# Kernel tuning notes

Measured on AMD Instinct MI355X. Metric: run time of the kernel, lower is better.

The kernel has to match this reference:

```python
import jax, jax.numpy as jnp
import numpy as np

IN_CH, OUT_CH, MINI = 1024, 1024, 8
GY, GX = OUT_CH // MINI, IN_CH // MINI  # 128, 128
BATCH = 32768


def setup_inputs() -> dict:
    key = jax.random.key(0)
    k1, k2 = jax.random.split(key)
    x = jax.random.normal(k1, (BATCH, IN_CH), dtype=jnp.float32)
    # kaiming-style init scale for the eigens parameter
    eigens = jax.random.normal(k2, (GY, GX, MINI), dtype=jnp.float32) * (2.0 / (GX * MINI)) ** 0.5
    return {"x": x, "eigens": eigens}


def reference(x, eigens):
    # Block-circulant linear: for each (y, x_blk) grid cell, circularly convolve
    # the length-MINI eigen vector with the corresponding input block, then sum
    # over input blocks. Done in the frequency domain (full FFT, matching
    # torch.rfft(..., onesided=False) + complex_mult + irfft in the original),
    # but with the redundant gridDim_y repeat fused into a complex einsum.
    gy, gx, k = eigens.shape
    xb = x.reshape(-1, gx, k)                      # [B, GX, K]
    f_e = jnp.fft.fft(eigens, axis=-1)             # [GY, GX, K] complex
    f_x = jnp.fft.fft(xb, axis=-1)                 # [B, GX, K] complex
    f_out = jnp.einsum('yxk,bxk->byk', f_e, f_x)   # elementwise mult + sum over GX
    out = jnp.fft.ifft(f_out, axis=-1).real.astype(x.dtype)  # [B, GY, K]
    return out.reshape(-1, gy * k)                 # [B, OUT_CH]
```

## Files before the change

kernel.cpp:

```cpp
#include <hip/hip_runtime.h>
#include <stdint.h>

#define M_BATCH 32768
#define N_OUT   1024
#define K_IN    1024

#define BM 128
#define BN 128
#define BK 64

typedef __attribute__((ext_vector_type(8))) short  short8;
typedef __attribute__((ext_vector_type(4))) float  f32x4;

__device__ __forceinline__ unsigned short f2bf(float f) {
    __bf16 h = (__bf16)f;
    return __builtin_bit_cast(unsigned short, h);
}

__global__ __launch_bounds__(256) void build_w(const float* __restrict__ eig,
                                               unsigned short* __restrict__ W) {
    int tid = blockIdx.x * 256 + threadIdx.x;
    int y  = tid >> 7;
    int xb = tid & 127;
    const float* e = eig + (size_t)((y << 7) + xb) * 8;
    f32x4 e0 = *reinterpret_cast<const f32x4*>(e);
    f32x4 e1 = *reinterpret_cast<const f32x4*>(e + 4);
    float ev[8] = {e0[0], e0[1], e0[2], e0[3], e1[0], e1[1], e1[2], e1[3]};
#pragma unroll
    for (int j = 0; j < 8; ++j) {
        alignas(16) unsigned short wv[8];
#pragma unroll
        for (int c = 0; c < 8; ++c) wv[c] = f2bf(ev[(j - c) & 7]);
        *reinterpret_cast<uint4*>(W + (size_t)(y * 8 + j) * K_IN + xb * 8) =
            *reinterpret_cast<const uint4*>(wv);
    }
}

__global__ __launch_bounds__(256) void gemm_bt(const float* __restrict__ A,
                                               const unsigned short* __restrict__ W,
                                               float* __restrict__ C) {
    __shared__ unsigned short Alds[BM * BK];
    __shared__ unsigned short Blds[BN * BK];

    const int bid  = blockIdx.x;
    const int swz  = (bid & 7) * 256 + (bid >> 3);
    const int nblk = swz & 7;
    const int mblk = swz >> 3;
    const int brow = mblk * BM;
    const int bcol = nblk * BN;

    const int tid  = threadIdx.x;
    const int lane = tid & 63;
    const int wv   = tid >> 6;
    const int wm   = wv >> 1;
    const int wn   = wv & 1;

    f32x4 acc[4][4];
    const f32x4 zero = {0.f, 0.f, 0.f, 0.f};
#pragma unroll
    for (int i = 0; i < 4; ++i)
#pragma unroll
        for (int j = 0; j < 4; ++j) acc[i][j] = zero;

    const int srow  = tid >> 3;
    const int sslot = tid & 7;
    const int sk8   = sslot ^ (srow & 7);
    const float*          Abase = A + (size_t)(brow + srow) * K_IN + sk8 * 8;
    const unsigned short* Wbase = W + (size_t)(bcol + srow) * K_IN + sk8 * 8;
    unsigned short* AldsW = Alds + srow * BK + sslot * 8;
    unsigned short* BldsW = Blds + srow * BK + sslot * 8;

    for (int kt = 0; kt < K_IN; kt += BK) {
        __syncthreads();
#pragma unroll
        for (int it = 0; it < 4; ++it) {
            const float* src = Abase + (size_t)it * 32 * K_IN + kt;
            f32x4 v0 = *reinterpret_cast<const f32x4*>(src);
            f32x4 v1 = *reinterpret_cast<const f32x4*>(src + 4);
            short8 b;
#pragma unroll
            for (int i = 0; i < 4; ++i) b[i]     = (short)f2bf(v0[i]);
#pragma unroll
            for (int i = 0; i < 4; ++i) b[i + 4] = (short)f2bf(v1[i]);
            *reinterpret_cast<short8*>(AldsW + it * 32 * BK) = b;
        }
#pragma unroll
        for (int it = 0; it < 4; ++it) {
            const unsigned short* src = Wbase + (size_t)it * 32 * K_IN + kt;
            short8 b = *reinterpret_cast<const short8*>(src);
            *reinterpret_cast<short8*>(BldsW + it * 32 * BK) = b;
        }
        __syncthreads();
#pragma unroll
        for (int ks = 0; ks < 2; ++ks) {
            short8 af[4], bfr[4];
            const int cb = ks * 4 + (lane >> 4);
#pragma unroll
            for (int mt = 0; mt < 4; ++mt) {
                int row  = wm * 64 + mt * 16 + (lane & 15);
                int slot = cb ^ (row & 7);
                af[mt] = *reinterpret_cast<const short8*>(Alds + row * BK + slot * 8);
            }
#pragma unroll
            for (int nt = 0; nt < 4; ++nt) {
                int row  = wn * 64 + nt * 16 + (lane & 15);
                int slot = cb ^ (row & 7);
                bfr[nt] = *reinterpret_cast<const short8*>(Blds + row * BK + slot * 8);
            }
#pragma unroll
            for (int mt = 0; mt < 4; ++mt)
#pragma unroll
                for (int nt = 0; nt < 4; ++nt)
                    acc[mt][nt] = __builtin_amdgcn_mfma_f32_16x16x32_bf16(
                        af[mt], bfr[nt], acc[mt][nt], 0, 0, 0);
        }
    }

#pragma unroll
    for (int mt = 0; mt < 4; ++mt) {
#pragma unroll
        for (int nt = 0; nt < 4; ++nt) {
            int col = bcol + wn * 64 + nt * 16 + (lane & 15);
#pragma unroll
            for (int r = 0; r < 4; ++r) {
                int row = brow + wm * 64 + mt * 16 + (lane >> 4) * 4 + r;
                C[(size_t)row * N_OUT + col] = acc[mt][nt][r];
            }
        }
    }
}

extern "C" void kernel_launch(void* const* d_in, const int* in_sizes, int n_in,
                              void* d_out, int out_size, void* d_ws, size_t ws_size,
                              hipStream_t stream) {
    const float* x   = (const float*)d_in[0];
    const float* eig = (const float*)d_in[1];
    float* out = (float*)d_out;
    unsigned short* W = (unsigned short*)d_ws;
    if (ws_size < (size_t)N_OUT * K_IN * sizeof(unsigned short)) return;

    hipLaunchKernelGGL(build_w, dim3((16384 + 255) / 256), dim3(256), 0, stream,
                       eig, W);
    hipLaunchKernelGGL(gemm_bt, dim3((M_BATCH / BM) * (N_OUT / BN)), dim3(256),
                       0, stream, x, W, out);
}
```

Baseline: 329.8 us.

## Pre-convert x to bf16 and load GEMM tiles directly into LDS

Adds a separate pass that converts x from fp32 to bf16 in workspace. A new GEMM kernel then uses global_load_lds to copy bf16 tiles for both operands straight into shared memory, replacing the register-staged fp32 load and in-loop conversion. This cuts the GEMM's A-operand traffic and its conversion work, at the cost of an extra full read and write of x. The path only runs when the workspace is large enough; otherwise it falls back to the old kernel.

New measurement: 298.2 us. -9.6%, faster.

```diff
diff --git a/kernel.cpp b/kernel.cpp
--- a/kernel.cpp
+++ b/kernel.cpp
@@ -15,6 +15,29 @@
 __device__ __forceinline__ unsigned short f2bf(float f) {
     __bf16 h = (__bf16)f;
     return __builtin_bit_cast(unsigned short, h);
+}
+
+typedef const __attribute__((address_space(1))) unsigned int* gas_ptr;
+typedef __attribute__((address_space(3))) unsigned int*       las_ptr;
+
+__device__ __forceinline__ void gload_lds16(const void* g, void* l) {
+    __builtin_amdgcn_global_load_lds((gas_ptr)g, (las_ptr)l, 16, 0, 0);
+}
+
+__global__ __launch_bounds__(256) void cvt_x(const float* __restrict__ x,
+                                             unsigned short* __restrict__ xb) {
+    const size_t total8 = (size_t)M_BATCH * K_IN / 8;
+    const size_t stride = (size_t)gridDim.x * 256;
+    for (size_t i = (size_t)blockIdx.x * 256 + threadIdx.x; i < total8; i += stride) {
+        f32x4 v0 = *reinterpret_cast<const f32x4*>(x + i * 8);
+        f32x4 v1 = *reinterpret_cast<const f32x4*>(x + i * 8 + 4);
+        short8 b;
+#pragma unroll
+        for (int j = 0; j < 4; ++j) b[j]     = (short)f2bf(v0[j]);
+#pragma unroll
+        for (int j = 0; j < 4; ++j) b[j + 4] = (short)f2bf(v1[j]);
+        *reinterpret_cast<short8*>(xb + i * 8) = b;
+    }
 }
 
 __global__ __launch_bounds__(256) void build_w(const float* __restrict__ eig,
@@ -36,6 +59,87 @@
     }
 }
 
+__global__ __launch_bounds__(256) void gemm_bf16(const unsigned short* __restrict__ A,
+                                                 const unsigned short* __restrict__ W,
+                                                 float* __restrict__ C) {
+    __shared__ unsigned short Alds[BM * BK];
+    __shared__ unsigned short Blds[BN * BK];
+
+    const int bid  = blockIdx.x;
+    const int swz  = (bid & 7) * 256 + (bid >> 3);
+    const int nblk = swz & 7;
+    const int mblk = swz >> 3;
+    const int brow = mblk * BM;
+    const int bcol = nblk * BN;
+
+    const int tid  = threadIdx.x;
+    const int lane = tid & 63;
+    const int wv   = tid >> 6;
+    const int wm   = wv >> 1;
+    const int wn   = wv & 1;
+
+    f32x4 acc[4][4];
+    const f32x4 zero = {0.f, 0.f, 0.f, 0.f};
+#pragma unroll
+    for (int i = 0; i < 4; ++i)
+#pragma unroll
+        for (int j = 0; j < 4; ++j) acc[i][j] = zero;
+
+    const int lrow = lane >> 3;
+    const int lchk = (lane & 7) ^ lrow;
+    const size_t arow0 = (size_t)(brow + wv * 32 + lrow);
+    const size_t brow0 = (size_t)(bcol + wv * 32 + lrow);
+    const unsigned short* Abase = A + arow0 * K_IN + lchk * 8;
+    const unsigned short* Bbase = W + brow0 * K_IN + lchk * 8;
+    unsigned short* AldsBase = Alds + wv * 2048;
+    unsigned short* BldsBase = Blds + wv * 2048;
+
+    for (int kt = 0; kt < K_IN; kt += BK) {
+        __syncthreads();
+#pragma unroll
+        for (int s = 0; s < 4; ++s) {
+            gload_lds16(Abase + (size_t)(s * 8) * K_IN + kt, AldsBase + s * 512);
+            gload_lds16(Bbase + (size_t)(s * 8) * K_IN + kt, BldsBase + s * 512);
+        }
+        __syncthreads();
+#pragma unroll
+        for (int ks = 0; ks < 2; ++ks) {
+            short8 af[4], bfr[4];
+            const int cb = ks * 4 + (lane >> 4);
+            const int sl = cb ^ (lane & 7);
+#pragma unroll
+            for (int mt = 0; mt < 4; ++mt) {
+                int row = wm * 64 + mt * 16 + (lane & 15);
+                af[mt] = *reinterpret_cast<const short8*>(Alds + row * BK + sl * 8);
+            }
+#pragma unroll
+            for (int nt = 0; nt < 4; ++nt) {
+                int row = wn * 64 + nt * 16 + (lane & 15);
+                bfr[nt] = *reinterpret_cast<const short8*>(Blds + row * BK + sl * 8);
+            }
+#pragma unroll
+            for (int mt = 0; mt < 4; ++mt)
+#pragma unroll
+                for (int nt = 0; nt < 4; ++nt)
+                    acc[mt][nt] = __builtin_amdgcn_mfma_f32_16x16x32_bf16(
+                        af[mt], bfr[nt], acc[mt][nt], 0, 0, 0);
+        }
+    }
+
+#pragma unroll
+    for (int mt = 0; mt < 4; ++mt) {
+#pragma unroll
+        for (int nt = 0; nt < 4; ++nt) {
+            int col = bcol + wn * 64 + nt * 16 + (lane & 15);
+#pragma unroll
+            for (int r = 0; r < 4; ++r) {
+                int row = brow + wm * 64 + mt * 16 + (lane >> 4) * 4 + r;
+                C[(size_t)row * N_OUT + col] = acc[mt][nt][r];
+            }
+        }
+    }
+}
+
 __global__ __launch_bounds__(256) void gemm_bt(const float* __restrict__ A,
                                                const unsigned short* __restrict__ W,
                                                float* __restrict__ C) {
@@ -136,11 +240,22 @@
     const float* x   = (const float*)d_in[0];
     const float* eig = (const float*)d_in[1];
     float* out = (float*)d_out;
-    unsigned short* W = (unsigned short*)d_ws;
-    if (ws_size < (size_t)N_OUT * K_IN * sizeof(unsigned short)) return;
-
-    hipLaunchKernelGGL(build_w, dim3((16384 + 255) / 256), dim3(256), 0, stream,
-                       eig, W);
-    hipLaunchKernelGGL(gemm_bt, dim3((M_BATCH / BM) * (N_OUT / BN)), dim3(256),
-                       0, stream, x, W, out);
-}
+
+    const size_t XB     = (size_t)M_BATCH * K_IN;
+    const size_t W_ELTS = (size_t)N_OUT * K_IN;
+    const size_t need   = XB * sizeof(unsigned short) + W_ELTS * sizeof(unsigned short);
+
+    if (ws_size >= need) {
+        unsigned short* xb = (unsigned short*)d_ws;
+        unsigned short* W  = (unsigned short*)d_ws + XB;
+        hipLaunchKernelGGL(cvt_x, dim3(2048), dim3(256), 0, stream, x, xb);
+        hipLaunchKernelGGL(build_w, dim3(64), dim3(256), 0, stream, eig, W);
+        hipLaunchKernelGGL(gemm_bf16, dim3((M_BATCH / BM) * (N_OUT / BN)), dim3(256),
+                           0, stream, xb, W, out);
+    } else if (ws_size >= W_ELTS * sizeof(unsigned short)) {
+        unsigned short* W = (unsigned short*)d_ws;
+        hipLaunchKernelGGL(build_w, dim3(64), dim3(256), 0, stream, eig, W);
+        hipLaunchKernelGGL(gemm_bt, dim3((M_BATCH / BM) * (N_OUT / BN)), dim3(256),
+                           0, stream, x, W, out);
+    }
+}
```

## Prefetch A tile into registers and stream W via direct global-to-LDS loads

Applied to the files above, without the earlier changes.

Restructures the GEMM main loop so the next fp32 A tile is loaded into registers while the current tile is converted and computed. The W tile now goes straight from global memory to LDS through global_load_lds, using a fixed per-wave layout. Explicit waitcnt, raw barriers and setprio around the MFMA block replace the __syncthreads pairs. The aim is to hide global load latency and overlap memory with MFMA, at the cost of more registers and hand-managed synchronisation that could race if the vmcnt count is wrong.

New measurement: 335.1 us. About the same (+1.6%).

```diff
diff --git a/kernel.cpp b/kernel.cpp
--- a/kernel.cpp
+++ b/kernel.cpp
@@ -8,6 +8,7 @@
 #define BM 128
 #define BN 128
 #define BK 64
+#define NT (K_IN / BK)
 
 typedef __attribute__((ext_vector_type(8))) short  short8;
 typedef __attribute__((ext_vector_type(4))) float  f32x4;
@@ -15,6 +16,13 @@
 __device__ __forceinline__ unsigned short f2bf(float f) {
     __bf16 h = (__bf16)f;
     return __builtin_bit_cast(unsigned short, h);
+}
+
+typedef const __attribute__((address_space(1))) unsigned int* gas_ptr;
+typedef __attribute__((address_space(3))) unsigned int*       las_ptr;
+
+__device__ __forceinline__ void gload_lds16(const void* g, void* l) {
+    __builtin_amdgcn_global_load_lds((gas_ptr)g, (las_ptr)l, 16, 0, 0);
 }
 
 __global__ __launch_bounds__(256) void build_w(const float* __restrict__ eig,
@@ -36,9 +44,9 @@
     }
 }
 
-__global__ __launch_bounds__(256) void gemm_bt(const float* __restrict__ A,
-                                               const unsigned short* __restrict__ W,
-                                               float* __restrict__ C) {
+__global__ __launch_bounds__(256) void gemm_fused(const float* __restrict__ A,
+                                                  const unsigned short* __restrict__ W,
+                                                  float* __restrict__ C) {
     __shared__ unsigned short Alds[BM * BK];
     __shared__ unsigned short Blds[BN * BK];
 
@@ -65,54 +73,78 @@
     const int srow  = tid >> 3;
     const int sslot = tid & 7;
     const int sk8   = sslot ^ (srow & 7);
-    const float*          Abase = A + (size_t)(brow + srow) * K_IN + sk8 * 8;
-    const unsigned short* Wbase = W + (size_t)(bcol + srow) * K_IN + sk8 * 8;
+    const float*    Af    = A + (size_t)(brow + srow) * K_IN + sk8 * 8;
     unsigned short* AldsW = Alds + srow * BK + sslot * 8;
-    unsigned short* BldsW = Blds + srow * BK + sslot * 8;
 
-    for (int kt = 0; kt < K_IN; kt += BK) {
-        __syncthreads();
+    const int lrow = lane >> 3;
+    const int lchk = (lane & 7) ^ lrow;
+    const unsigned short* Bbase = W + (size_t)(bcol + wv * 32 + lrow) * K_IN + lchk * 8;
+    unsigned short* BldsBase = Blds + wv * 2048;
+
+    f32x4 aPre[4][2];
+#pragma unroll
+    for (int it = 0; it < 4; ++it) {
+        const float* s = Af + (size_t)it * 32 * K_IN;
+        aPre[it][0] = *reinterpret_cast<const f32x4*>(s);
+        aPre[it][1] = *reinterpret_cast<const f32x4*>(s + 4);
+    }
+
+    for (int t = 0; t < NT; ++t) {
+        const int kt  = t * BK;
+        const int ktn = (kt + BK) & (K_IN - 1);
+
+        __builtin_amdgcn_s_barrier();
+        __builtin_amdgcn_sched_barrier(0);
+
+#pragma unroll
+        for (int s = 0; s < 4; ++s)
+            gload_lds16(Bbase + (size_t)(s * 8) * K_IN + kt, BldsBase + s * 512);
+        asm volatile("" ::: "memory");
+
 #pragma unroll
         for (int it = 0; it < 4; ++it) {
-            const float* src = Abase + (size_t)it * 32 * K_IN + kt;
-            f32x4 v0 = *reinterpret_cast<const f32x4*>(src);
-            f32x4 v1 = *reinterpret_cast<const f32x4*>(src + 4);
             short8 b;
 #pragma unroll
-            for (int i = 0; i < 4; ++i) b[i]     = (short)f2bf(v0[i]);
+            for (int i = 0; i < 4; ++i) b[i]     = (short)f2bf(aPre[it][0][i]);
 #pragma unroll
-            for (int i = 0; i < 4; ++i) b[i + 4] = (short)f2bf(v1[i]);
+            for (int i = 0; i < 4; ++i) b[i + 4] = (short)f2bf(aPre[it][1][i]);
             *reinterpret_cast<short8*>(AldsW + it * 32 * BK) = b;
         }
+
 #pragma unroll
         for (int it = 0; it < 4; ++it) {
-            const unsigned short* src = Wbase + (size_t)it * 32 * K_IN + kt;
-            short8 b = *reinterpret_cast<const short8*>(src);
-            *reinterpret_cast<short8*>(BldsW + it * 32 * BK) = b;
+            const float* s = Af + (size_t)it * 32 * K_IN + ktn;
+            aPre[it][0] = *reinterpret_cast<const f32x4*>(s);
+            aPre[it][1] = *reinterpret_cast<const f32x4*>(s + 4);
         }
-        __syncthreads();
+
+        asm volatile("s_waitcnt vmcnt(8) lgkmcnt(0)" ::: "memory");
+        __builtin_amdgcn_s_barrier();
+        __builtin_amdgcn_sched_barrier(0);
+
 #pragma unroll
         for (int ks = 0; ks < 2; ++ks) {
             short8 af[4], bfr[4];
             const int cb = ks * 4 + (lane >> 4);
+            const int sl = cb ^ (lane & 7);
 #pragma unroll
             for (int mt = 0; mt < 4; ++mt) {
-                int row  = wm * 64 + mt * 16 + (lane & 15);
-                int slot = cb ^ (row & 7);
-                af[mt] = *reinterpret_cast<const short8*>(Alds + row * BK + slot * 8);
+                int row = wm * 64 + mt * 16 + (lane & 15);
+                af[mt] = *reinterpret_cast<const short8*>(Alds + row * BK + sl * 8);
             }
 #pragma unroll
             for (int nt = 0; nt < 4; ++nt) {
-                int row  = wn * 64 + nt * 16 + (lane & 15);
-                int slot = cb ^ (row & 7);
-                bfr[nt] = *reinterpret_cast<const short8*>(Blds + row * BK + slot * 8);
+                int row = wn * 64 + nt * 16 + (lane & 15);
+                bfr[nt] = *reinterpret_cast<const short8*>(Blds + row * BK + sl * 8);
             }
+            __builtin_amdgcn_s_setprio(1);
 #pragma unroll
             for (int mt = 0; mt < 4; ++mt)
 #pragma unroll
                 for (int nt = 0; nt < 4; ++nt)
                     acc[mt][nt] = __builtin_amdgcn_mfma_f32_16x16x32_bf16(
                         af[mt], bfr[nt], acc[mt][nt], 0, 0, 0);
+            __builtin_amdgcn_s_setprio(0);
         }
     }
 
@@ -136,11 +168,12 @@
     const float* x   = (const float*)d_in[0];
     const float* eig = (const float*)d_in[1];
     float* out = (float*)d_out;
+
+    const size_t W_ELTS = (size_t)N_OUT * K_IN;
+    if (ws_size < W_ELTS * sizeof(unsigned short)) return;
     unsigned short* W = (unsigned short*)d_ws;
-    if (ws_size < (size_t)N_OUT * K_IN * sizeof(unsigned short)) return;
 
-    hipLaunchKernelGGL(build_w, dim3((16384 + 255) / 256), dim3(256), 0, stream,
-                       eig, W);
-    hipLaunchKernelGGL(gemm_bt, dim3((M_BATCH / BM) * (N_OUT / BN)), dim3(256),
+    hipLaunchKernelGGL(build_w, dim3(64), dim3(256), 0, stream, eig, W);
+    hipLaunchKernelGGL(gemm_fused, dim3((M_BATCH / BM) * (N_OUT / BN)), dim3(256),
                        0, stream, x, W, out);
 }
```
